# Kernel tuning notes

Measured on AMD Instinct MI355X. Metric: run time of the kernel, lower is better.

## Reference

```python
import jax, jax.numpy as jnp
import numpy as np

N = 100000
F_IN = 128
HID = 128
NCLS = 40
NEG_SLOPE = 0.2
BN_EPS = 1e-5


def setup_inputs() -> dict:
    key = jax.random.key(0)
    ks = jax.random.split(key, 16)
    x = jax.random.normal(ks[0], (N, F_IN), dtype=jnp.float32)
    # self-loop-free random edges: dst = (src + 1 + r) % N
    E = 1600000
    src = jax.random.randint(ks[1], (E,), 0, N)
    off = jax.random.randint(ks[2], (E,), 1, N)
    dst = (src + off) % N
    edge_index = jnp.stack([src, dst]).astype(jnp.int64)

    def glorot(k, shape):
        fan = shape[0] + shape[-1]
        s = jnp.sqrt(6.0 / fan)
        return jax.random.uniform(k, shape, jnp.float32, -s, s)

    params = {
        'W1': glorot(ks[3], (F_IN, HID)),
        'as1': glorot(ks[4], (HID,)), 'ad1': glorot(ks[5], (HID,)),
        'b1': jnp.zeros((HID,), jnp.float32),
        'g1': jnp.ones((HID,), jnp.float32), 'beta1': jnp.zeros((HID,), jnp.float32),
        'W2': glorot(ks[6], (HID, HID)),
        'as2': glorot(ks[7], (HID,)), 'ad2': glorot(ks[8], (HID,)),
        'b2': jnp.zeros((HID,), jnp.float32),
        'g2': jnp.ones((HID,), jnp.float32), 'beta2': jnp.zeros((HID,), jnp.float32),
        'Wc': glorot(ks[9], (HID, NCLS)),
        'bc': jnp.zeros((NCLS,), jnp.float32),
    }
    return {'x': x, 'edge_index': edge_index, **params}


def _gat_conv(h_in, src, dst, W, a_src, a_dst, bias):
    # heads=1, concat=False -> single head, mean over heads is identity
    h = h_in @ W                               # [N, C]
    alpha_s = h @ a_src                        # [N]
    alpha_d = h @ a_dst                        # [N]
    alpha = alpha_s[src] + alpha_d[dst]        # [E] edge score
    alpha = jax.nn.leaky_relu(alpha, NEG_SLOPE)
    # segment softmax over destination node neighborhoods
    m = jax.ops.segment_max(alpha, dst, num_segments=N)
    e = jnp.exp(alpha - m[dst])
    s = jax.ops.segment_sum(e, dst, num_segments=N)
    alpha = e / s[dst]
    msg = h[src] * alpha[:, None]              # [E, C]
    out = jax.ops.segment_sum(msg, dst, num_segments=N)
    return out + bias


def _batchnorm(x, gamma, beta):
    mu = jnp.mean(x, axis=0)
    var = jnp.mean(jnp.square(x - mu), axis=0)  # biased, as torch BN training
    return (x - mu) * jax.lax.rsqrt(var + BN_EPS) * gamma + beta


def reference(x, edge_index, W1, as1, ad1, b1, g1, beta1,
              W2, as2, ad2, b2, g2, beta2, Wc, bc):
    src, dst = edge_index[0], edge_index[1]
    # add self loops (input edges are guaranteed self-loop-free)
    loop = jnp.arange(N, dtype=src.dtype)
    src = jnp.concatenate([src, loop])
    dst = jnp.concatenate([dst, loop])

    h = _gat_conv(x, src, dst, W1, as1, ad1, b1)
    h = jax.nn.relu(_batchnorm(h, g1, beta1))
    h = _gat_conv(h, src, dst, W2, as2, ad2, b2)
    h = jax.nn.relu(_batchnorm(h, g2, beta2))
    return h @ Wc + bc
```

## Files before the change

### kernel.cpp

```cpp
#include <hip/hip_runtime.h>
#include <hip/hip_fp16.h>
#include <math.h>


#define CDIM 128
#define NCLS_ 40
#define NEG_SLOPE_ 0.2f
#define BN_EPS_ 1e-5f
#define BRNG 256
#define BCAP 6144
#define EPB 16

using short8  = __attribute__((ext_vector_type(8))) short;
using short4v = __attribute__((ext_vector_type(4))) short;
using f32x4   = __attribute__((ext_vector_type(4))) float;

static __device__ __forceinline__ float lrelu(float a) {
    return a > 0.f ? a : NEG_SLOPE_ * a;
}
static __device__ __forceinline__ short f2bf(float f) {
    unsigned u = __float_as_uint(f);
    u += 0x7fffu + ((u >> 16) & 1u);
    return (short)(u >> 16);
}
static __device__ __forceinline__ float bf_lo(unsigned u) { return __uint_as_float(u << 16); }
static __device__ __forceinline__ float bf_hi(unsigned u) { return __uint_as_float(u & 0xffff0000u); }
static __device__ __forceinline__ __half2 u2h2(unsigned u) { return __builtin_bit_cast(__half2, u); }
static __device__ __forceinline__ unsigned h22u(__half2 h) { return __builtin_bit_cast(unsigned, h); }

__global__ void k_setup(int* bcur, float* bnsum, int NB, int n, int E, int* offs,
                        const float* __restrict__ W1, const float* __restrict__ W2,
                        const float* __restrict__ Wc,
                        const float* __restrict__ as1, const float* __restrict__ ad1,
                        const float* __restrict__ as2, const float* __restrict__ ad2,
                        short* __restrict__ Wt1, short* __restrict__ Wt2,
                        short* __restrict__ Wtc,
                        short* __restrict__ wsd1, short* __restrict__ wsd2) {
    int i = blockIdx.x * blockDim.x + threadIdx.x;
    if (i < NB) bcur[i] = 0;
    if (i < 512) bnsum[i] = 0.f;
    if (i == 0) offs[n] = E + n;
    if (i < 128 * 128) {
        int k = i >> 7, nn = i & 127;
        Wt1[nn * 128 + k] = f2bf(W1[i]);
        Wt2[nn * 128 + k] = f2bf(W2[i]);
    }
    if (i < 48 * 128) {
        int nn = i >> 7, k = i & 127;
        Wtc[i] = (nn < NCLS_) ? f2bf(Wc[k * NCLS_ + nn]) : (short)0;
    }
    if (i < 128) {
        float s1 = 0.f, d1 = 0.f, s2 = 0.f, d2 = 0.f;
        for (int nn2 = 0; nn2 < 128; nn2++) {
            float w1v = W1[i * 128 + nn2], w2v = W2[i * 128 + nn2];
            s1 = fmaf(w1v, as1[nn2], s1); d1 = fmaf(w1v, ad1[nn2], d1);
            s2 = fmaf(w2v, as2[nn2], s2); d2 = fmaf(w2v, ad2[nn2], d2);
        }
        wsd1[i] = f2bf(s1); wsd1[128 + i] = f2bf(d1);
        wsd2[i] = f2bf(s2); wsd2[128 + i] = f2bf(d2);
    }
}

__global__ __launch_bounds__(256) void k_binA(
    const int* __restrict__ src, const int* __restrict__ dst, int E,
    int* __restrict__ bcur, uint2* __restrict__ bucket, int NB)
{
    __shared__ int hist[400];
    __shared__ int base[400];
    int t = threadIdx.x;
    long e0 = (long)blockIdx.x * (256 * EPB) + t;

    for (int i = t; i < NB; i += 256) hist[i] = 0;
    __syncthreads();

    int sv[EPB], dv[EPB];
    #pragma unroll
    for (int i = 0; i < EPB; i++) {
        long e = e0 + (long)i * 256;
        if (e < E) {
            sv[i] = src[e]; dv[i] = dst[e];
            atomicAdd(&hist[dv[i] >> 8], 1);
        } else dv[i] = -1;
    }
    __syncthreads();

    for (int i = t; i < NB; i += 256) {
        int h = hist[i];
        base[i] = (h > 0) ? atomicAdd(&bcur[i], h) : 0;
    }
    __syncthreads();
    for (int i = t; i < NB; i += 256) hist[i] = 0;
    __syncthreads();

    #pragma unroll
    for (int i = 0; i < EPB; i++) {
        if (dv[i] >= 0) {
            int b = dv[i] >> 8;
            int pos = base[b] + atomicAdd(&hist[b], 1);
            if (pos < BCAP)
                bucket[(size_t)b * BCAP + pos] =
                    make_uint2((unsigned)sv[i], (unsigned)dv[i]);
        }
    }
}

__global__ __launch_bounds__(256) void k_fillB(
    const uint2* __restrict__ bucket, const int* __restrict__ bcur,
    int n, int NB, int* __restrict__ offs, int* __restrict__ csr)
{
    __shared__ int hist[256];
    __shared__ int scanb[256];
    __shared__ int cur[256];
    __shared__ int buf[BCAP + BRNG];
    int b = blockIdx.x, t = threadIdx.x;
    int node0 = b << 8;
    int nodesIn = min(BRNG, n - node0);
    int cnt = min(bcur[b], BCAP);
    const uint2* mybkt = bucket + (size_t)b * BCAP;

    int part = 0;
    for (int j = t; j < b; j += 256) part += min(bcur[j], BCAP);
    scanb[t] = part; __syncthreads();
    for (int s2 = 128; s2 > 0; s2 >>= 1) {
        if (t < s2) scanb[t] += scanb[t + s2];
        __syncthreads();
    }
    int base = scanb[0] + node0;
    __syncthreads();

    hist[t] = 0; __syncthreads();
    for (int e2 = t; e2 < cnt; e2 += 256)
        atomicAdd(&hist[mybkt[e2].y & 255], 1);
    __syncthreads();

    int v = hist[t] + ((t < nodesIn) ? 1 : 0);
    scanb[t] = v; __syncthreads();
    for (int d = 1; d < 256; d <<= 1) {
        int x2 = (t >= d) ? scanb[t - d] : 0;
        __syncthreads();
        scanb[t] += x2;
        __syncthreads();
    }
    int lo = scanb[t] - v;
    if (t < nodesIn) {
        offs[node0 + t] = base + lo;
        buf[lo] = node0 + t;
        cur[t] = lo + 1;
    }
    __syncthreads();

    for (int e2 = t; e2 < cnt; e2 += 256) {
        uint2 ed = mybkt[e2];
        int pos = atomicAdd(&cur[ed.y & 255], 1);
        buf[pos] = (int)ed.x;
    }
    __syncthreads();

    int tot = cnt + nodesIn;
    for (int j2 = t; j2 < tot; j2 += 256) csr[base + j2] = buf[j2];
}

__global__ __launch_bounds__(256) void k_gemm_mfma(
    const float* __restrict__ Xf, const unsigned* __restrict__ Xb,
    const short* __restrict__ Wt, const short* __restrict__ wsd,
    const float* __restrict__ bnsum, const float* __restrict__ gamma,
    const float* __restrict__ beta, float invn,
    short* __restrict__ Hh, float* __restrict__ alpha_s, float* __restrict__ alpha_d,
    int n, int fuse)
{
    __shared__ short As[64 * 128];
    __shared__ short Bs[128 * 128];
    __shared__ short wl[256];
    int t = threadIdx.x;
    int row0 = blockIdx.x * 64;

    for (int j = 0; j < 8; j++) {
        int idx = j * 256 + t;
        int nn = idx >> 4, cc = idx & 15;
        *(short8*)(Bs + nn * 128 + cc * 8) = *(const short8*)(Wt + nn * 128 + cc * 8);
    }
    if (t < 256) wl[t] = wsd[t];
    float4 sc4 = make_float4(1.f, 1.f, 1.f, 1.f);
    float4 sh4 = make_float4(0.f, 0.f, 0.f, 0.f);
    if (fuse) {
        int cb = (t & 31) * 4;
        float4 s0 = *(const float4*)(bnsum + cb);
        float4 s1 = *(const float4*)(bnsum + 128 + cb);
        float4 gm = *(const float4*)(gamma + cb);
        float4 bt = *(const float4*)(beta + cb);
        float mean, var;
        mean = s0.x * invn; var = fmaxf(s1.x * invn - mean * mean, 0.f);
        sc4.x = gm.x * rsqrtf(var + BN_EPS_); sh4.x = bt.x - mean * sc4.x;
        mean = s0.y * invn; var = fmaxf(s1.y * invn - mean * mean, 0.f);
        sc4.y = gm.y * rsqrtf(var + BN_EPS_); sh4.y = bt.y - mean * sc4.y;
        mean = s0.z * invn; var = fmaxf(s1.z * invn - mean * mean, 0.f);
        sc4.z = gm.z * rsqrtf(var + BN_EPS_); sh4.z = bt.z - mean * sc4.z;
        mean = s0.w * invn; var = fmaxf(s1.w * invn - mean * mean, 0.f);
        sc4.w = gm.w * rsqrtf(var + BN_EPS_); sh4.w = bt.w - mean * sc4.w;
    }
    for (int j = 0; j < 8; j++) {
        int idx = j * 256 + t;
        int r = idx >> 5, k4 = idx & 31;
        int gr = row0 + r;
        float4 xv = make_float4(0.f, 0.f, 0.f, 0.f);
        if (fuse) {
            if (gr < n) {
                uint2 u = *(const uint2*)(Xb + (size_t)gr * 64 + k4 * 2);
                xv.x = bf_lo(u.x); xv.y = bf_hi(u.x);
                xv.z = bf_lo(u.y); xv.w = bf_hi(u.y);
            }
            xv.x = fmaxf(fmaf(xv.x, sc4.x, sh4.x), 0.f);
            xv.y = fmaxf(fmaf(xv.y, sc4.y, sh4.y), 0.f);
            xv.z = fmaxf(fmaf(xv.z, sc4.z, sh4.z), 0.f);
            xv.w = fmaxf(fmaf(xv.w, sc4.w, sh4.w), 0.f);
        } else {
            if (gr < n) xv = *(const float4*)(Xf + (size_t)gr * CDIM + k4 * 4);
        }
        short4v o;
        o.x = f2bf(xv.x); o.y = f2bf(xv.y); o.z = f2bf(xv.z); o.w = f2bf(xv.w);
        *(short4v*)(As + r * 128 + k4 * 4) = o;
    }
    __syncthreads();

    int w = t >> 6, lane = t & 63, q = lane >> 4, c = lane & 15;
    f32x4 zero = {0.f, 0.f, 0.f, 0.f};
    f32x4 acc[4][2];
    f32x4 acc_a = zero;
    for (int i = 0; i < 4; i++) { acc[i][0] = zero; acc[i][1] = zero; }

    for (int ks = 0; ks < 4; ks++) {
        int k0 = ks * 32 + q * 8;
        short8 a0 = *(short8*)(As + (c) * 128 + k0);
        short8 a1 = *(short8*)(As + (16 + c) * 128 + k0);
        short8 a2 = *(short8*)(As + (32 + c) * 128 + k0);
        short8 a3 = *(short8*)(As + (48 + c) * 128 + k0);
        short8 b0 = *(short8*)(Bs + (w * 32 + c) * 128 + k0);
        short8 b1 = *(short8*)(Bs + (w * 32 + 16 + c) * 128 + k0);
        acc[0][0] = __builtin_amdgcn_mfma_f32_16x16x32_bf16(a0, b0, acc[0][0], 0, 0, 0);
        acc[1][0] = __builtin_amdgcn_mfma_f32_16x16x32_bf16(a1, b0, acc[1][0], 0, 0, 0);
        acc[2][0] = __builtin_amdgcn_mfma_f32_16x16x32_bf16(a2, b0, acc[2][0], 0, 0, 0);
        acc[3][0] = __builtin_amdgcn_mfma_f32_16x16x32_bf16(a3, b0, acc[3][0], 0, 0, 0);
        acc[0][1] = __builtin_amdgcn_mfma_f32_16x16x32_bf16(a0, b1, acc[0][1], 0, 0, 0);
        acc[1][1] = __builtin_amdgcn_mfma_f32_16x16x32_bf16(a1, b1, acc[1][1], 0, 0, 0);
        acc[2][1] = __builtin_amdgcn_mfma_f32_16x16x32_bf16(a2, b1, acc[2][1], 0, 0, 0);
        acc[3][1] = __builtin_amdgcn_mfma_f32_16x16x32_bf16(a3, b1, acc[3][1], 0, 0, 0);

        short8 ba;
        #pragma unroll
        for (int jj = 0; jj < 8; jj++) {
            short vs = wl[k0 + jj], vd = wl[128 + k0 + jj];
            ba[jj] = (c == 0) ? vs : ((c == 1) ? vd : (short)0);
        }
        short8 aw = (w == 0) ? a0 : ((w == 1) ? a1 : ((w == 2) ? a2 : a3));
        acc_a = __builtin_amdgcn_mfma_f32_16x16x32_bf16(aw, ba, acc_a, 0, 0, 0);
    }

    __syncthreads();

    short* Hs = As;
    #pragma unroll
    for (int mt = 0; mt < 4; mt++)
        #pragma unroll
        for (int nt = 0; nt < 2; nt++)
            #pragma unroll
            for (int r = 0; r < 4; r++)
                Hs[(mt * 16 + q * 4 + r) * 128 + w * 32 + nt * 16 + c] =
                    (short)__half_as_ushort(__float2half_rn(acc[mt][nt][r]));

    if (c < 2) {
        #pragma unroll
        for (int r = 0; r < 4; r++) {
            int row = row0 + w * 16 + q * 4 + r;
            if (row < n) {
                if (c == 0) alpha_s[row] = acc_a[r];
                else        alpha_d[row] = acc_a[r];
            }
        }
    }
    __syncthreads();

    for (int j = 0; j < 4; j++) {
        int idx = j * 256 + t;
        int r = idx >> 4, cc = idx & 15;
        int gr = row0 + r;
        if (gr < n)
            *(short8*)(Hh + (size_t)gr * 128 + cc * 8) = *(short8*)(Hs + r * 128 + cc * 8);
    }
}

__global__ __launch_bounds__(256) void k_agg(
    const unsigned* __restrict__ Hh, const int* __restrict__ offs,
    const int* __restrict__ csr, const float* __restrict__ alpha_s,
    const float* __restrict__ alpha_d, const float* __restrict__ bias,
    unsigned* __restrict__ Ob, int n)
{
    int i = blockIdx.x * 4 + (threadIdx.x >> 6);
    int lane = threadIdx.x & 63;
    if (i >= n) return;
    int o0 = offs[i], o1 = offs[i + 1];
    float adi = alpha_d[i];

    float m = -1e30f;
    float se = 0.f;
    __half2 acc2 = __floats2half2_rn(0.f, 0.f);

    for (int c0 = o0; c0 < o1; c0 += 64) {
        int j = c0 + lane;
        int cnt = min(64, o1 - c0);
        int sj = (j < o1) ? csr[j] : 0;

        unsigned ua[8], ub[8], uc[8];
        #pragma unroll
        for (int q = 0; q < 8; q++) {
            int s = __builtin_amdgcn_readlane(sj, q);
            ua[q] = Hh[(size_t)(unsigned)s * 64 + lane];
        }
        if (cnt > 8) {
            #pragma unroll
            for (int q = 0; q < 8; q++) {
                int s = __builtin_amdgcn_readlane(sj, 8 + q);
                ub[q] = Hh[(size_t)(unsigned)s * 64 + lane];
            }
        }
        if (cnt > 16) {
            #pragma unroll
            for (int q = 0; q < 8; q++) {
                int s = __builtin_amdgcn_readlane(sj, 16 + q);
                uc[q] = Hh[(size_t)(unsigned)s * 64 + lane];
            }
        }

        float a = (j < o1) ? lrelu(alpha_s[sj] + adi) : -1e30f;
        float cm = a;
        #pragma unroll
        for (int o = 32; o > 0; o >>= 1) cm = fmaxf(cm, __shfl_xor(cm, o));
        if (cm > m) {
            float r = __expf(m - cm);
            se *= r;
            acc2 = __hmul2(acc2, __float2half2_rn(r));
            m = cm;
        }
        float wl2 = (j < o1) ? __expf(a - m) : 0.f;
        se += wl2;
        int wli = (int)h22u(__float2half2_rn(wl2));

        for (int b = 0; b < cnt; b += 24) {
            #pragma unroll
            for (int q = 0; q < 8; q++) {
                int wq = __builtin_amdgcn_readlane(wli, b + q);
                acc2 = __hfma2(u2h2(ua[q]), u2h2((unsigned)wq), acc2);
            }
            if (b + 24 < cnt) {
                #pragma unroll
                for (int q = 0; q < 8; q++) {
                    int s = __builtin_amdgcn_readlane(sj, b + 24 + q);
                    ua[q] = Hh[(size_t)(unsigned)s * 64 + lane];
                }
            }
            if (b + 8 < cnt) {
                #pragma unroll
                for (int q = 0; q < 8; q++) {
                    int wq = __builtin_amdgcn_readlane(wli, b + 8 + q);
                    acc2 = __hfma2(u2h2(ub[q]), u2h2((unsigned)wq), acc2);
                }
                if (b + 32 < cnt) {
                    #pragma unroll
                    for (int q = 0; q < 8; q++) {
                        int s = __builtin_amdgcn_readlane(sj, b + 32 + q);
                        ub[q] = Hh[(size_t)(unsigned)s * 64 + lane];
                    }
                }
                if (b + 16 < cnt) {
                    #pragma unroll
                    for (int q = 0; q < 8; q++) {
                        int wq = __builtin_amdgcn_readlane(wli, b + 16 + q);
                        acc2 = __hfma2(u2h2(uc[q]), u2h2((unsigned)wq), acc2);
                    }
                    if (b + 40 < cnt) {
                        #pragma unroll
                        for (int q = 0; q < 8; q++) {
                            int s = __builtin_amdgcn_readlane(sj, b + 40 + q);
                            uc[q] = Hh[(size_t)(unsigned)s * 64 + lane];
                        }
                    }
                }
            }
        }
    }

    #pragma unroll
    for (int o = 32; o > 0; o >>= 1) se += __shfl_xor(se, o);
    float inv = 1.f / se;
    float2 af = __half22float2(acc2);
    float2 b2 = *(const float2*)(bias + lane * 2);
    float rx = fmaf(af.x, inv, b2.x);
    float ry = fmaf(af.y, inv, b2.y);
    unsigned pack = ((unsigned)(unsigned short)f2bf(ry) << 16) |
                    (unsigned)(unsigned short)f2bf(rx);
    Ob[(size_t)i * 64 + lane] = pack;
}

__global__ void k_bnstats(const unsigned* __restrict__ Hb, int n, float* __restrict__ sums) {
    __shared__ float red[4][64][4];
    int w = threadIdx.x & 63;
    int g = threadIdx.x >> 6;
    float slo = 0.f, shi = 0.f, qlo = 0.f, qhi = 0.f;
    for (int r = blockIdx.x * 4 + g; r < n; r += gridDim.x * 4) {
        unsigned u = Hb[(size_t)r * 64 + w];
        float lo = bf_lo(u), hi = bf_hi(u);
        slo += lo; shi += hi; qlo += lo * lo; qhi += hi * hi;
    }
    red[g][w][0] = slo; red[g][w][1] = shi; red[g][w][2] = qlo; red[g][w][3] = qhi;
    __syncthreads();
    if (threadIdx.x < 64) {
        int w2 = threadIdx.x;
        float s0 = 0.f, s1 = 0.f, s2 = 0.f, s3 = 0.f;
        for (int gg = 0; gg < 4; gg++) {
            s0 += red[gg][w2][0]; s1 += red[gg][w2][1];
            s2 += red[gg][w2][2]; s3 += red[gg][w2][3];
        }
        atomicAdd(&sums[2 * w2], s0);
        atomicAdd(&sums[2 * w2 + 1], s1);
        atomicAdd(&sums[128 + 2 * w2], s2);
        atomicAdd(&sums[128 + 2 * w2 + 1], s3);
    }
}

__global__ __launch_bounds__(256) void k_cls(
    const unsigned* __restrict__ G, const short* __restrict__ Wtc,
    const float* __restrict__ bc, const float* __restrict__ bnsum,
    const float* __restrict__ gamma, const float* __restrict__ beta, float invn,
    float* __restrict__ out, int n)
{
    __shared__ short As[64 * 128];
    __shared__ short Bs[48 * 128];
    int t = threadIdx.x;
    int row0 = blockIdx.x * 64;

    for (int j = 0; j < 3; j++) {
        int idx = j * 256 + t;
        *(short8*)(Bs + idx * 8) = *(const short8*)(Wtc + idx * 8);
    }
    float4 sc4, sh4;
    {
        int cb = (t & 31) * 4;
        float4 s0 = *(const float4*)(bnsum + cb);
        float4 s1 = *(const float4*)(bnsum + 128 + cb);
        float4 gm = *(const float4*)(gamma + cb);
        float4 bt = *(const float4*)(beta + cb);
        float mean, var;
        mean = s0.x * invn; var = fmaxf(s1.x * invn - mean * mean, 0.f);
        sc4.x = gm.x * rsqrtf(var + BN_EPS_); sh4.x = bt.x - mean * sc4.x;
        mean = s0.y * invn; var = fmaxf(s1.y * invn - mean * mean, 0.f);
        sc4.y = gm.y * rsqrtf(var + BN_EPS_); sh4.y = bt.y - mean * sc4.y;
        mean = s0.z * invn; var = fmaxf(s1.z * invn - mean * mean, 0.f);
        sc4.z = gm.z * rsqrtf(var + BN_EPS_); sh4.z = bt.z - mean * sc4.z;
        mean = s0.w * invn; var = fmaxf(s1.w * invn - mean * mean, 0.f);
        sc4.w = gm.w * rsqrtf(var + BN_EPS_); sh4.w = bt.w - mean * sc4.w;
    }
    for (int j = 0; j < 8; j++) {
        int idx = j * 256 + t;
        int r = idx >> 5, k4 = idx & 31;
        int gr = row0 + r;
        float4 xv = make_float4(0.f, 0.f, 0.f, 0.f);
        if (gr < n) {
            uint2 u = *(const uint2*)(G + (size_t)gr * 64 + k4 * 2);
            xv.x = bf_lo(u.x); xv.y = bf_hi(u.x);
            xv.z = bf_lo(u.y); xv.w = bf_hi(u.y);
        }
        xv.x = fmaxf(fmaf(xv.x, sc4.x, sh4.x), 0.f);
        xv.y = fmaxf(fmaf(xv.y, sc4.y, sh4.y), 0.f);
        xv.z = fmaxf(fmaf(xv.z, sc4.z, sh4.z), 0.f);
        xv.w = fmaxf(fmaf(xv.w, sc4.w, sh4.w), 0.f);
        short4v o;
        o.x = f2bf(xv.x); o.y = f2bf(xv.y); o.z = f2bf(xv.z); o.w = f2bf(xv.w);
        *(short4v*)(As + r * 128 + k4 * 4) = o;
    }
    __syncthreads();

    int w = t >> 6, lane = t & 63, q = lane >> 4, c = lane & 15;
    f32x4 zero = {0.f, 0.f, 0.f, 0.f};
    f32x4 acc[3] = {zero, zero, zero};
    for (int ks = 0; ks < 4; ks++) {
        int k0 = ks * 32 + q * 8;
        short8 a  = *(short8*)(As + (w * 16 + c) * 128 + k0);
        short8 b0 = *(short8*)(Bs + (c) * 128 + k0);
        short8 b1 = *(short8*)(Bs + (16 + c) * 128 + k0);
        short8 b2 = *(short8*)(Bs + (32 + c) * 128 + k0);
        acc[0] = __builtin_amdgcn_mfma_f32_16x16x32_bf16(a, b0, acc[0], 0, 0, 0);
        acc[1] = __builtin_amdgcn_mfma_f32_16x16x32_bf16(a, b1, acc[1], 0, 0, 0);
        acc[2] = __builtin_amdgcn_mfma_f32_16x16x32_bf16(a, b2, acc[2], 0, 0, 0);
    }
    float bc0 = bc[c], bc1 = bc[16 + c], bc2 = (c < 8) ? bc[32 + c] : 0.f;
    #pragma unroll
    for (int r = 0; r < 4; r++) {
        int row = row0 + w * 16 + q * 4 + r;
        if (row < n) {
            out[(size_t)row * NCLS_ + c]      = acc[0][r] + bc0;
            out[(size_t)row * NCLS_ + 16 + c] = acc[1][r] + bc1;
            if (c < 8) out[(size_t)row * NCLS_ + 32 + c] = acc[2][r] + bc2;
        }
    }
}

extern "C" void kernel_launch(void* const* d_in, const int* in_sizes, int n_in,
                              void* d_out, int out_size, void* d_ws, size_t ws_size,
                              hipStream_t stream)
{
    const float* x   = (const float*)d_in[0];
    const int*   ei  = (const int*)d_in[1];
    const float* W1  = (const float*)d_in[2];
    const float* as1 = (const float*)d_in[3];
    const float* ad1 = (const float*)d_in[4];
    const float* b1  = (const float*)d_in[5];
    const float* g1  = (const float*)d_in[6];
    const float* be1 = (const float*)d_in[7];
    const float* W2  = (const float*)d_in[8];
    const float* as2 = (const float*)d_in[9];
    const float* ad2 = (const float*)d_in[10];
    const float* b2  = (const float*)d_in[11];
    const float* g2  = (const float*)d_in[12];
    const float* be2 = (const float*)d_in[13];
    const float* Wc  = (const float*)d_in[14];
    const float* bc  = (const float*)d_in[15];
    float* out = (float*)d_out;

    int n = in_sizes[0] / CDIM;
    int E = in_sizes[1] / 2;
    const int* src = ei;
    const int* dst = ei + E;
    float invn = 1.f / (float)n;
    int NB = (n + BRNG - 1) / BRNG;

    char* p = (char*)d_ws;
    auto alloc = [&p](size_t bytes) { char* q = p; p += (bytes + 63) & ~(size_t)63; return q; };
    short*    Hh      = (short*)alloc((size_t)n * CDIM * sizeof(short));
    unsigned* bufB    = (unsigned*)alloc((size_t)n * 64 * sizeof(unsigned));
    float*    alpha_s = (float*)alloc((size_t)n * sizeof(float));
    float*    alpha_d = (float*)alloc((size_t)n * sizeof(float));
    float*    bnsum   = (float*)alloc(512 * sizeof(float));
    short*    Wt1     = (short*)alloc(128 * 128 * sizeof(short));
    short*    Wt2     = (short*)alloc(128 * 128 * sizeof(short));
    short*    Wtc     = (short*)alloc(48 * 128 * sizeof(short));
    short*    wsd1    = (short*)alloc(256 * sizeof(short));
    short*    wsd2    = (short*)alloc(256 * sizeof(short));
    int*      bcurs   = (int*)alloc((size_t)NB * sizeof(int));
    int*      offs    = (int*)alloc((size_t)(n + 1) * sizeof(int));
    uint2*    bucket  = (uint2*)alloc((size_t)NB * BCAP * sizeof(uint2));
    int*      csr     = (int*)alloc((size_t)(E + n) * sizeof(int));

    k_setup<<<dim3(64), dim3(256), 0, stream>>>(bcurs, bnsum, NB, n, E, offs,
                                                W1, W2, Wc, as1, ad1, as2, ad2,
                                                Wt1, Wt2, Wtc, wsd1, wsd2);
    k_binA<<<dim3((E + 4095) / 4096), dim3(256), 0, stream>>>(src, dst, E, bcurs, bucket, NB);
    k_fillB<<<dim3(NB), dim3(256), 0, stream>>>(bucket, bcurs, n, NB, offs, csr);

    dim3 ggrid((n + 63) / 64);
    dim3 wgrid((n + 3) / 4);

    k_gemm_mfma<<<ggrid, 256, 0, stream>>>(x, nullptr, Wt1, wsd1, nullptr, nullptr,
                                           nullptr, invn, Hh, alpha_s, alpha_d, n, 0);
    k_agg<<<wgrid, 256, 0, stream>>>((const unsigned*)Hh, offs, csr, alpha_s, alpha_d,
                                     b1, bufB, n);
    k_bnstats<<<dim3(256), dim3(256), 0, stream>>>(bufB, n, bnsum);

    k_gemm_mfma<<<ggrid, 256, 0, stream>>>(nullptr, bufB, Wt2, wsd2, bnsum, g1,
                                           be1, invn, Hh, alpha_s, alpha_d, n, 1);
    k_agg<<<wgrid, 256, 0, stream>>>((const unsigned*)Hh, offs, csr, alpha_s, alpha_d,
                                     b2, bufB, n);
    k_bnstats<<<dim3(256), dim3(256), 0, stream>>>(bufB, n, bnsum + 256);

    k_cls<<<ggrid, 256, 0, stream>>>(bufB, Wtc, bc, bnsum + 256, g2, be2, invn, out, n);
}
```

Measured before the change: 436.1 us.

## Merge first-layer GEMM with edge binning into one heterogeneous launch

Combines the layer-1 feature GEMM and the edge bucketing pass into a single kernel whose blocks split by index: the first blocks do the GEMM, the rest do binning. The two independent stages can then overlap on the GPU instead of running back to back, and one launch is saved. The second-layer GEMM loses its runtime fuse flag. Shared memory is a union sized by the GEMM tile, so binning blocks reserve more LDS than they use, which may lower their occupancy.

New measurement: 424.7 us. 2.6% less time.

```diff
diff --git a/kernel.cpp b/kernel.cpp
--- a/kernel.cpp
+++ b/kernel.cpp
@@ -61,46 +61,146 @@
     }
 }
 
-__global__ __launch_bounds__(256) void k_binA(
+__global__ __launch_bounds__(256) void k_pre(
+    const float* __restrict__ Xf, const short* __restrict__ Wt,
+    const short* __restrict__ wsd, short* __restrict__ Hh,
+    float* __restrict__ alpha_s, float* __restrict__ alpha_d, int n, int gemmN,
     const int* __restrict__ src, const int* __restrict__ dst, int E,
     int* __restrict__ bcur, uint2* __restrict__ bucket, int NB)
 {
-    __shared__ int hist[400];
-    __shared__ int base[400];
+    __shared__ union {
+        struct { short As[64 * 128]; short Bs[128 * 128]; short wl[256]; } g;
+        struct { int hist[400]; int base[400]; } b;
+    } sm;
     int t = threadIdx.x;
-    long e0 = (long)blockIdx.x * (256 * EPB) + t;
-
-    for (int i = t; i < NB; i += 256) hist[i] = 0;
-    __syncthreads();
-
-    int sv[EPB], dv[EPB];
+
+    if (blockIdx.x >= gemmN) {
+        int bid = blockIdx.x - gemmN;
+        int* hist = sm.b.hist;
+        int* base = sm.b.base;
+        long e0 = (long)bid * (256 * EPB) + t;
+
+        for (int i = t; i < NB; i += 256) hist[i] = 0;
+        __syncthreads();
+
+        int sv[EPB], dv[EPB];
+        #pragma unroll
+        for (int i = 0; i < EPB; i++) {
+            long e = e0 + (long)i * 256;
+            if (e < E) {
+                sv[i] = src[e]; dv[i] = dst[e];
+                atomicAdd(&hist[dv[i] >> 8], 1);
+            } else dv[i] = -1;
+        }
+        __syncthreads();
+
+        for (int i = t; i < NB; i += 256) {
+            int h = hist[i];
+            base[i] = (h > 0) ? atomicAdd(&bcur[i], h) : 0;
+        }
+        __syncthreads();
+        for (int i = t; i < NB; i += 256) hist[i] = 0;
+        __syncthreads();
+
+        #pragma unroll
+        for (int i = 0; i < EPB; i++) {
+            if (dv[i] >= 0) {
+                int b = dv[i] >> 8;
+                int pos = base[b] + atomicAdd(&hist[b], 1);
+                if (pos < BCAP)
+                    bucket[(size_t)b * BCAP + pos] =
+                        make_uint2((unsigned)sv[i], (unsigned)dv[i]);
+            }
+        }
+        return;
+    }
+
+    short* As = sm.g.As;
+    short* Bs = sm.g.Bs;
+    short* wl = sm.g.wl;
+    int row0 = blockIdx.x * 64;
+
+    for (int j = 0; j < 8; j++) {
+        int idx = j * 256 + t;
+        int nn = idx >> 4, cc = idx & 15;
+        *(short8*)(Bs + nn * 128 + cc * 8) = *(const short8*)(Wt + nn * 128 + cc * 8);
+    }
+    if (t < 256) wl[t] = wsd[t];
+    for (int j = 0; j < 8; j++) {
+        int idx = j * 256 + t;
+        int r = idx >> 5, k4 = idx & 31;
+        int gr = row0 + r;
+        float4 xv = make_float4(0.f, 0.f, 0.f, 0.f);
+        if (gr < n) xv = *(const float4*)(Xf + (size_t)gr * CDIM + k4 * 4);
+        short4v o;
+        o.x = f2bf(xv.x); o.y = f2bf(xv.y); o.z = f2bf(xv.z); o.w = f2bf(xv.w);
+        *(short4v*)(As + r * 128 + k4 * 4) = o;
+    }
+    __syncthreads();
+
+    int w = t >> 6, lane = t & 63, q = lane >> 4, c = lane & 15;
+    f32x4 zero = {0.f, 0.f, 0.f, 0.f};
+    f32x4 acc[4][2];
+    f32x4 acc_a = zero;
+    for (int i = 0; i < 4; i++) { acc[i][0] = zero; acc[i][1] = zero; }
+
+    for (int ks = 0; ks < 4; ks++) {
+        int k0 = ks * 32 + q * 8;
+        short8 a0 = *(short8*)(As + (c) * 128 + k0);
+        short8 a1 = *(short8*)(As + (16 + c) * 128 + k0);
+        short8 a2 = *(short8*)(As + (32 + c) * 128 + k0);
+        short8 a3 = *(short8*)(As + (48 + c) * 128 + k0);
+        short8 b0 = *(short8*)(Bs + (w * 32 + c) * 128 + k0);
+        short8 b1 = *(short8*)(Bs + (w * 32 + 16 + c) * 128 + k0);
+        acc[0][0] = __builtin_amdgcn_mfma_f32_16x16x32_bf16(a0, b0, acc[0][0], 0, 0, 0);
+        acc[1][0] = __builtin_amdgcn_mfma_f32_16x16x32_bf16(a1, b0, acc[1][0], 0, 0, 0);
+        acc[2][0] = __builtin_amdgcn_mfma_f32_16x16x32_bf16(a2, b0, acc[2][0], 0, 0, 0);
+        acc[3][0] = __builtin_amdgcn_mfma_f32_16x16x32_bf16(a3, b0, acc[3][0], 0, 0, 0);
+        acc[0][1] = __builtin_amdgcn_mfma_f32_16x16x32_bf16(a0, b1, acc[0][1], 0, 0, 0);
+        acc[1][1] = __builtin_amdgcn_mfma_f32_16x16x32_bf16(a1, b1, acc[1][1], 0, 0, 0);
+        acc[2][1] = __builtin_amdgcn_mfma_f32_16x16x32_bf16(a2, b1, acc[2][1], 0, 0, 0);
+        acc[3][1] = __builtin_amdgcn_mfma_f32_16x16x32_bf16(a3, b1, acc[3][1], 0, 0, 0);
+
+        short8 ba;
+        #pragma unroll
+        for (int jj = 0; jj < 8; jj++) {
+            short vs = wl[k0 + jj], vd = wl[128 + k0 + jj];
+            ba[jj] = (c == 0) ? vs : ((c == 1) ? vd : (short)0);
+        }
+        short8 aw = (w == 0) ? a0 : ((w == 1) ? a1 : ((w == 2) ? a2 : a3));
+        acc_a = __builtin_amdgcn_mfma_f32_16x16x32_bf16(aw, ba, acc_a, 0, 0, 0);
+    }
+
+    __syncthreads();
+
+    short* Hs = As;
     #pragma unroll
-    for (int i = 0; i < EPB; i++) {
-        long e = e0 + (long)i * 256;
-        if (e < E) {
-            sv[i] = src[e]; dv[i] = dst[e];
-            atomicAdd(&hist[dv[i] >> 8], 1);
-        } else dv[i] = -1;
-    }
-    __syncthreads();
-
-    for (int i = t; i < NB; i += 256) {
-        int h = hist[i];
-        base[i] = (h > 0) ? atomicAdd(&bcur[i], h) : 0;
-    }
-    __syncthreads();
-    for (int i = t; i < NB; i += 256) hist[i] = 0;
-    __syncthreads();
-
-    #pragma unroll
-    for (int i = 0; i < EPB; i++) {
-        if (dv[i] >= 0) {
-            int b = dv[i] >> 8;
-            int pos = base[b] + atomicAdd(&hist[b], 1);
-            if (pos < BCAP)
-                bucket[(size_t)b * BCAP + pos] =
-                    make_uint2((unsigned)sv[i], (unsigned)dv[i]);
-        }
+    for (int mt = 0; mt < 4; mt++)
+        #pragma unroll
+        for (int nt = 0; nt < 2; nt++)
+            #pragma unroll
+            for (int r = 0; r < 4; r++)
+                Hs[(mt * 16 + q * 4 + r) * 128 + w * 32 + nt * 16 + c] =
+                    (short)__half_as_ushort(__float2half_rn(acc[mt][nt][r]));
+
+    if (c < 2) {
+        #pragma unroll
+        for (int r = 0; r < 4; r++) {
+            int row = row0 + w * 16 + q * 4 + r;
+            if (row < n) {
+                if (c == 0) alpha_s[row] = acc_a[r];
+                else        alpha_d[row] = acc_a[r];
+            }
+        }
+    }
+    __syncthreads();
+
+    for (int j = 0; j < 4; j++) {
+        int idx = j * 256 + t;
+        int r = idx >> 4, cc = idx & 15;
+        int gr = row0 + r;
+        if (gr < n)
+            *(short8*)(Hh + (size_t)gr * 128 + cc * 8) = *(short8*)(Hs + r * 128 + cc * 8);
     }
 }
 
@@ -161,12 +261,12 @@
 }
 
 __global__ __launch_bounds__(256) void k_gemm_mfma(
-    const float* __restrict__ Xf, const unsigned* __restrict__ Xb,
-    const short* __restrict__ Wt, const short* __restrict__ wsd,
+    const unsigned* __restrict__ Xb, const short* __restrict__ Wt,
+    const short* __restrict__ wsd,
     const float* __restrict__ bnsum, const float* __restrict__ gamma,
     const float* __restrict__ beta, float invn,
     short* __restrict__ Hh, float* __restrict__ alpha_s, float* __restrict__ alpha_d,
-    int n, int fuse)
+    int n)
 {
     __shared__ short As[64 * 128];
     __shared__ short Bs[128 * 128];
@@ -180,9 +280,8 @@
         *(short8*)(Bs + nn * 128 + cc * 8) = *(const short8*)(Wt + nn * 128 + cc * 8);
     }
     if (t < 256) wl[t] = wsd[t];
-    float4 sc4 = make_float4(1.f, 1.f, 1.f, 1.f);
-    float4 sh4 = make_float4(0.f, 0.f, 0.f, 0.f);
-    if (fuse) {
+    float4 sc4, sh4;
+    {
         int cb = (t & 31) * 4;
         float4 s0 = *(const float4*)(bnsum + cb);
         float4 s1 = *(const float4*)(bnsum + 128 + cb);
@@ -203,19 +302,15 @@
         int r = idx >> 5, k4 = idx & 31;
         int gr = row0 + r;
         float4 xv = make_float4(0.f, 0.f, 0.f, 0.f);
-        if (fuse) {
-            if (gr < n) {
-                uint2 u = *(const uint2*)(Xb + (size_t)gr * 64 + k4 * 2);
-                xv.x = bf_lo(u.x); xv.y = bf_hi(u.x);
-                xv.z = bf_lo(u.y); xv.w = bf_hi(u.y);
-            }
-            xv.x = fmaxf(fmaf(xv.x, sc4.x, sh4.x), 0.f);
-            xv.y = fmaxf(fmaf(xv.y, sc4.y, sh4.y), 0.f);
-            xv.z = fmaxf(fmaf(xv.z, sc4.z, sh4.z), 0.f);
-            xv.w = fmaxf(fmaf(xv.w, sc4.w, sh4.w), 0.f);
-        } else {
-            if (gr < n) xv = *(const float4*)(Xf + (size_t)gr * CDIM + k4 * 4);
-        }
+        if (gr < n) {
+            uint2 u = *(const uint2*)(Xb + (size_t)gr * 64 + k4 * 2);
+            xv.x = bf_lo(u.x); xv.y = bf_hi(u.x);
+            xv.z = bf_lo(u.y); xv.w = bf_hi(u.y);
+        }
+        xv.x = fmaxf(fmaf(xv.x, sc4.x, sh4.x), 0.f);
+        xv.y = fmaxf(fmaf(xv.y, sc4.y, sh4.y), 0.f);
+        xv.z = fmaxf(fmaf(xv.z, sc4.z, sh4.z), 0.f);
+        xv.w = fmaxf(fmaf(xv.w, sc4.w, sh4.w), 0.f);
         short4v o;
         o.x = f2bf(xv.x); o.y = f2bf(xv.y); o.z = f2bf(xv.z); o.w = f2bf(xv.w);
         *(short4v*)(As + r * 128 + k4 * 4) = o;
@@ -552,20 +647,24 @@
     k_setup<<<dim3(64), dim3(256), 0, stream>>>(bcurs, bnsum, NB, n, E, offs,
                                                 W1, W2, Wc, as1, ad1, as2, ad2,
                                                 Wt1, Wt2, Wtc, wsd1, wsd2);
-    k_binA<<<dim3((E + 4095) / 4096), dim3(256), 0, stream>>>(src, dst, E, bcurs, bucket, NB);
+
+    int gemmN = (n + 63) / 64;
+    int binN  = (E + 4095) / 4096;
+    k_pre<<<dim3(gemmN + binN), dim3(256), 0, stream>>>(
+        x, Wt1, wsd1, Hh, alpha_s, alpha_d, n, gemmN,
+        src, dst, E, bcurs, bucket, NB);
+
     k_fillB<<<dim3(NB), dim3(256), 0, stream>>>(bucket, bcurs, n, NB, offs, csr);
 
-    dim3 ggrid((n + 63) / 64);
+    dim3 ggrid(gemmN);
     dim3 wgrid((n + 3) / 4);
 
-    k_gemm_mfma<<<ggrid, 256, 0, stream>>>(x, nullptr, Wt1, wsd1, nullptr, nullptr,
-                                           nullptr, invn, Hh, alpha_s, alpha_d, n, 0);
     k_agg<<<wgrid, 256, 0, stream>>>((const unsigned*)Hh, offs, csr, alpha_s, alpha_d,
                                      b1, bufB, n);
     k_bnstats<<<dim3(256), dim3(256), 0, stream>>>(bufB, n, bnsum);
 
-    k_gemm_mfma<<<ggrid, 256, 0, stream>>>(nullptr, bufB, Wt2, wsd2, bnsum, g1,
-                                           be1, invn, Hh, alpha_s, alpha_d, n, 1);
+    k_gemm_mfma<<<ggrid, 256, 0, stream>>>(bufB, Wt2, wsd2, bnsum, g1, be1,
+                                           invn, Hh, alpha_s, alpha_d, n);
     k_agg<<<wgrid, 256, 0, stream>>>((const unsigned*)Hh, offs, csr, alpha_s, alpha_d,
                                      b2, bufB, n);
     k_bnstats<<<dim3(256), dim3(256), 0, stream>>>(bufB, n, bnsum + 256);
```
